# Optimization experiments

Measured on AMD Instinct MI355X. Metric: run time of the kernel, lower is better.

Reference implementation:

```python
import jax, jax.numpy as jnp
import numpy as np

B, S, D = 2, 2048, 1024
H, A = 16, 64  # num_heads, attention_dim


def setup_inputs() -> dict:
    key = jax.random.key(0)
    ks = jax.random.split(key, 9)
    sd = D ** -0.5
    so = (H * A) ** -0.5
    return {
        "x": jax.random.normal(ks[0], (B, S, D), dtype=jnp.float32),
        "Wq": jax.random.normal(ks[1], (D, H * A), dtype=jnp.float32) * sd,
        "bq": jnp.zeros((H * A,), dtype=jnp.float32),
        "Wk": jax.random.normal(ks[2], (D, H * A), dtype=jnp.float32) * sd,
        "bk": jnp.zeros((H * A,), dtype=jnp.float32),
        "Wv": jax.random.normal(ks[3], (D, H * A), dtype=jnp.float32) * sd,
        "bv": jnp.zeros((H * A,), dtype=jnp.float32),
        "Wo": jax.random.normal(ks[4], (H * A, D), dtype=jnp.float32) * so,
        "bo": jnp.zeros((D,), dtype=jnp.float32),
    }


def reference(x, Wq, bq, Wk, bk, Wv, bv, Wo, bo):
    b, s, _ = x.shape
    # project and split heads: [b, s, H, A]
    q = (x @ Wq + bq).reshape(b, s, H, A)
    k = (x @ Wk + bk).reshape(b, s, H, A)
    v = (x @ Wv + bv).reshape(b, s, H, A)
    # scores [b, H, s, s]
    scores = jnp.einsum("bqhd,bkhd->bhqk", q, k) / jnp.sqrt(jnp.float32(A))
    weights = jax.nn.softmax(scores, axis=-1)
    attended = jnp.einsum("bhqk,bkhd->bqhd", weights, v).reshape(b, s, H * A)
    return attended @ Wo + bo
```

## Files before the change

### kernel.cpp

```cpp
#include <hip/hip_runtime.h>
#include <hip/hip_bf16.h>

typedef __attribute__((ext_vector_type(8))) short bf16x8;
typedef __attribute__((ext_vector_type(4))) float f32x4;

#define LOG2E 1.44269504088896f

extern "C" __device__ float __ocml_native_exp2_f32(float);

__device__ __forceinline__ unsigned short f2bf(float f) {
    union { float f; unsigned int u; } v; v.f = f;
    unsigned int r = v.u + 0x7FFF + ((v.u >> 16) & 1);
    return (unsigned short)(r >> 16);
}

__device__ __forceinline__ unsigned int pk_bf16(float lo, float hi) {
    unsigned int r;
    asm("v_cvt_pk_bf16_f32 %0, %1, %2" : "=v"(r) : "v"(lo), "v"(hi));
    return r;
}

typedef __attribute__((address_space(3))) unsigned int lds_uint;
typedef __attribute__((address_space(1))) const unsigned int glob_uint;
__device__ __forceinline__ void gl2lds16(const void* g, void* l) {
    __builtin_amdgcn_global_load_lds((glob_uint*)g, (lds_uint*)l, 16, 0, 0);
}

#define SYNC(vm)                                                             \
    asm volatile("s_waitcnt vmcnt(" #vm ")\n\ts_waitcnt lgkmcnt(0)" ::: "memory"); \
    __builtin_amdgcn_s_barrier();                                            \
    asm volatile("" ::: "memory")

__global__ __launch_bounds__(256) void cvt_bf16(const float* __restrict__ in,
                                                unsigned int* __restrict__ out, int n4) {
    int i = blockIdx.x * 256 + threadIdx.x;
    if (i >= n4) return;
    float4 v = ((const float4*)in)[i];
    uint2 o;
    o.x = pk_bf16(v.x, v.y);
    o.y = pk_bf16(v.z, v.w);
    ((uint2*)out)[i] = o;
}

__global__ __launch_bounds__(256) void transpose4_bf16(
    const float* __restrict__ w0, const float* __restrict__ w1,
    const float* __restrict__ w2, const float* __restrict__ w3,
    unsigned short* __restrict__ o0, unsigned short* __restrict__ o1,
    unsigned short* __restrict__ o2, unsigned short* __restrict__ o3) {
    const int z = blockIdx.z;
    const float* in = (z == 0) ? w0 : (z == 1) ? w1 : (z == 2) ? w2 : w3;
    unsigned short* out = (z == 0) ? o0 : (z == 1) ? o1 : (z == 2) ? o2 : o3;
    __shared__ float t[32][33];
    int tx = threadIdx.x & 31, ty = threadIdx.x >> 5;
    int r0 = blockIdx.y * 32, c0 = blockIdx.x * 32;
    for (int i = 0; i < 32; i += 8)
        t[ty + i][tx] = in[(size_t)(r0 + ty + i) * 1024 + c0 + tx];
    __syncthreads();
    for (int i = 0; i < 32; i += 8)
        out[(size_t)(c0 + ty + i) * 1024 + r0 + tx] = f2bf(t[tx][ty + i]);
}

__device__ __forceinline__ void gemm_core(const short* __restrict__ A,
                                          const short* __restrict__ BT,
                                          int K, int bm0, int bn0,
                                          short* sm, f32x4 acc[4][4]) {
    const int tid = threadIdx.x;
    const int lane = tid & 63;
    const int w = tid >> 6;
    const int wr0 = (w >> 1) * 64;
    const int wc0 = (w & 1) * 64;
    const int l15 = lane & 15, quad = lane >> 4;
    const int sr = lane >> 2;
    const int slog = (lane & 3) ^ (sr & 3) ^ (sr >> 2);

#pragma unroll
    for (int i = 0; i < 4; i++)
#pragma unroll
        for (int j = 0; j < 4; j++) acc[i][j] = (f32x4)0.f;

    const short* sp[4];
    int sdo[4];
#pragma unroll
    for (int i = 0; i < 4; i++) {
        int c = w * 4 + i;
        sp[i] = (c < 8) ? A + (size_t)(bm0 + c * 16 + sr) * K + slog * 8
                        : BT + (size_t)(bn0 + (c - 8) * 16 + sr) * K + slog * 8;
        sdo[i] = c * 512;
    }
    auto stage = [&](int buf) {
        short* bb = sm + buf * 8192;
#pragma unroll
        for (int i = 0; i < 4; i++) {
            gl2lds16(sp[i], bb + sdo[i]);
            sp[i] += 32;
        }
    };
    const int ph = (quad ^ (l15 & 3) ^ (l15 >> 2)) * 8;
    auto loadf = [&](bf16x8* af, bf16x8* bfr, int buf) {
        const short* Ab = sm + buf * 8192;
        const short* Bb = Ab + 4096;
#pragma unroll
        for (int im = 0; im < 4; im++)
            af[im] = *(const bf16x8*)&Ab[(wr0 + im * 16 + l15) * 32 + ph];
#pragma unroll
        for (int in = 0; in < 4; in++)
            bfr[in] = *(const bf16x8*)&Bb[(wc0 + in * 16 + l15) * 32 + ph];
        __builtin_amdgcn_sched_barrier(0);
    };
    auto computef = [&](const bf16x8* af, const bf16x8* bfr) {
        __builtin_amdgcn_s_setprio(1);
#pragma unroll
        for (int im = 0; im < 4; im++)
#pragma unroll
            for (int in = 0; in < 4; in++)
                acc[im][in] = __builtin_amdgcn_mfma_f32_16x16x32_bf16(af[im], bfr[in], acc[im][in], 0, 0, 0);
        __builtin_amdgcn_s_setprio(0);
    };

    stage(0); stage(1);
    asm volatile("s_waitcnt vmcnt(4)" ::: "memory");
    __builtin_amdgcn_s_barrier();
    asm volatile("" ::: "memory");

    bf16x8 aA[4], bA[4], aB[4], bB[4];
    loadf(aA, bA, 0);

    const int nt = K >> 5;
    int bs = 2, rb = 1;
    for (int t = 0; t < nt - 2; t += 2) {
        stage(bs); bs = (bs == 2) ? 0 : bs + 1;
        SYNC(4);
        loadf(aB, bB, rb); rb = (rb == 2) ? 0 : rb + 1;
        computef(aA, bA);
        stage(bs); bs = (bs == 2) ? 0 : bs + 1;
        SYNC(4);
        loadf(aA, bA, rb); rb = (rb == 2) ? 0 : rb + 1;
        computef(aB, bB);
    }
    SYNC(0);
    loadf(aB, bB, rb);
    computef(aA, bA);
    computef(aB, bB);
}

__global__ __launch_bounds__(256, 3) void gemm_qkv(
    const short* __restrict__ xb,
    const short* __restrict__ wqT, const short* __restrict__ wkT, const short* __restrict__ wvT,
    const float* __restrict__ bq, const float* __restrict__ bk, const float* __restrict__ bv,
    unsigned short* __restrict__ qb, unsigned short* __restrict__ kb, unsigned short* __restrict__ vTb) {
    __shared__ short sm[24576];
    const int z = blockIdx.z;
    const short* Amat = (z == 2) ? wvT : xb;
    const short* Bmat = (z == 0) ? wqT : (z == 1) ? wkT : xb;
    const float* bias = (z == 0) ? bq : (z == 1) ? bk : bv;
    const float scl = (z == 0) ? 0.125f * LOG2E : 1.f;
    const int bm0 = (z == 2) ? blockIdx.y * 128 : blockIdx.x * 128;
    const int bn0 = (z == 2) ? blockIdx.x * 128 : blockIdx.y * 128;
    f32x4 acc[4][4];
    gemm_core(Amat, Bmat, 1024, bm0, bn0, sm, acc);
    const int lane = threadIdx.x & 63, w = threadIdx.x >> 6;
    const int wr0 = (w >> 1) * 64, wc0 = (w & 1) * 64, l15 = lane & 15, quad = lane >> 4;
    if (z == 2) {
        for (int im = 0; im < 4; im++)
            for (int in = 0; in < 4; in++)
                for (int r = 0; r < 4; r++) {
                    int rowa = bm0 + wr0 + im * 16 + quad * 4 + r;
                    int colg = bn0 + wc0 + in * 16 + l15;
                    unsigned short ov = f2bf(acc[im][in][r] + bias[rowa]);
                    int b = colg >> 11, s = colg & 2047;
                    vTb[(size_t)b * 2097152 + (size_t)rowa * 2048 + s] = ov;
                }
    } else {
        for (int im = 0; im < 4; im++)
            for (int in = 0; in < 4; in++)
                for (int r = 0; r < 4; r++) {
                    int rowg = bm0 + wr0 + im * 16 + quad * 4 + r;
                    int colg = bn0 + wc0 + in * 16 + l15;
                    unsigned short ov = f2bf((acc[im][in][r] + bias[colg]) * scl);
                    int b = rowg >> 11, s = rowg & 2047;
                    int h = colg >> 6, a = colg & 63;
                    int bh = b * 16 + h;
                    if (z == 0) qb[((size_t)bh * 2048 + s) * 64 + a] = ov;
                    else        kb[((size_t)bh * 2048 + s) * 64 + a] = ov;
                }
    }
}

__global__ __launch_bounds__(256, 3) void gemm_out(
    const short* __restrict__ att, const short* __restrict__ woT,
    const float* __restrict__ bo, float* __restrict__ out) {
    __shared__ short sm[24576];
    const int bm0 = blockIdx.x * 128, bn0 = blockIdx.y * 128;
    f32x4 acc[4][4];
    gemm_core(att, woT, 1024, bm0, bn0, sm, acc);
    const int lane = threadIdx.x & 63, w = threadIdx.x >> 6;
    const int wr0 = (w >> 1) * 64, wc0 = (w & 1) * 64, l15 = lane & 15, quad = lane >> 4;
    for (int im = 0; im < 4; im++)
        for (int in = 0; in < 4; in++)
            for (int r = 0; r < 4; r++) {
                int rowg = bm0 + wr0 + im * 16 + quad * 4 + r;
                int colg = bn0 + wc0 + in * 16 + l15;
                out[(size_t)rowg * 1024 + colg] = acc[im][in][r] + bo[colg];
            }
}

__global__ __launch_bounds__(256, 2) void flash_attn(
    const unsigned short* __restrict__ qb, const unsigned short* __restrict__ kb,
    const unsigned short* __restrict__ vTb, unsigned short* __restrict__ att) {
    __shared__ short Ks[4][4096];
    __shared__ short Vs[4][4096];
    const int tid = threadIdx.x, lane = tid & 63, w = tid >> 6;
    const int l15 = lane & 15, quad = lane >> 4;
    const int q0 = blockIdx.x * 128;
    const int bh = blockIdx.y;
    const size_t qkbase = (size_t)bh * 2048 * 64;
    const size_t vbase = (size_t)bh * 64 * 2048;
    const int sr = lane >> 3;
    const int slog = (lane & 7) ^ sr;
    const int l7 = l15 & 7;

    const unsigned short* sgp;
    int sgstep, sgr;
    short* sgb;
    if (w < 2) {
        sgp = kb + qkbase + (size_t)(w * 32 + sr) * 64 + slog * 8;
        sgstep = 4096; sgr = 512;
        sgb = &Ks[0][0] + w * 2048;
    } else {
        sgp = vTb + vbase + (size_t)((w - 2) * 32 + sr) * 2048 + slog * 8;
        sgstep = 64; sgr = 16384;
        sgb = &Vs[0][0] + (w - 2) * 2048;
    }
    auto stage_tile = [&](int buf) {
        short* sd = sgb + buf * 4096;
        gl2lds16(sgp, sd);
        gl2lds16(sgp + sgr, sd + 512);
        gl2lds16(sgp + 2 * sgr, sd + 1024);
        gl2lds16(sgp + 3 * sgr, sd + 1536);
        sgp += sgstep;
    };

    const int wq0 = w * 32;
    const int c0 = (quad ^ l7) * 8, c1 = c0 ^ 32;
    const int fb = l15 * 64;

    const unsigned short* qrow = qb + qkbase + (size_t)(q0 + wq0 + l15) * 64 + quad * 8;
    bf16x8 aq00 = *(const bf16x8*)qrow;
    bf16x8 aq01 = *(const bf16x8*)(qrow + 32);
    bf16x8 aq10 = *(const bf16x8*)(qrow + 1024);
    bf16x8 aq11 = *(const bf16x8*)(qrow + 1024 + 32);

    stage_tile(0); stage_tile(1); stage_tile(2);
    asm volatile("s_waitcnt vmcnt(8)" ::: "memory");
    __builtin_amdgcn_s_barrier();
    asm volatile("" ::: "memory");

    f32x4 o0[4], o1[4];
#pragma unroll
    for (int dt = 0; dt < 4; dt++) { o0[dt] = (f32x4)0.f; o1[dt] = (f32x4)0.f; }
    f32x4 ls0 = (f32x4)0.f, ls1 = (f32x4)0.f;

    auto load_frags = [&](bf16x8* kf, bf16x8* vf, int buf) {
        const short* Kb = &Ks[0][0] + buf * 4096;
        const short* Vb = &Vs[0][0] + buf * 4096;
#pragma unroll
        for (int t = 0; t < 4; t++) {
            kf[2 * t]     = *(const bf16x8*)(Kb + fb + c0 + t * 1024);
            kf[2 * t + 1] = *(const bf16x8*)(Kb + fb + c1 + t * 1024);
            vf[2 * t]     = *(const bf16x8*)(Vb + fb + c0 + t * 1024);
            vf[2 * t + 1] = *(const bf16x8*)(Vb + fb + c1 + t * 1024);
        }
        __builtin_amdgcn_sched_barrier(0);
    };

    auto smax = [&](f32x4 (&sc)[4], f32x4& lsr, bf16x8 (&bp)[2]) {
#pragma unroll
        for (int t = 0; t < 4; t++) {
#pragma unroll
            for (int r = 0; r < 4; r++) sc[t][r] = __ocml_native_exp2_f32(sc[t][r]);
            lsr += sc[t];
        }
#pragma unroll
        for (int t2 = 0; t2 < 2; t2++) {
            unsigned pa = pk_bf16(sc[2 * t2][0], sc[2 * t2][1]);
            unsigned pb = pk_bf16(sc[2 * t2][2], sc[2 * t2][3]);
            unsigned pc = pk_bf16(sc[2 * t2 + 1][0], sc[2 * t2 + 1][1]);
            unsigned pd = pk_bf16(sc[2 * t2 + 1][2], sc[2 * t2 + 1][3]);
            asm("v_permlane32_swap_b32 %0, %1" : "+v"(pa), "+v"(pc));
            asm("v_permlane32_swap_b32 %0, %1" : "+v"(pb), "+v"(pd));
            asm("v_permlane16_swap_b32 %0, %1" : "+v"(pa), "+v"(pc));
            asm("v_permlane16_swap_b32 %0, %1" : "+v"(pb), "+v"(pd));
            union { unsigned u[4]; bf16x8 v; } cvt;
            cvt.u[0] = pa; cvt.u[1] = pb; cvt.u[2] = pc; cvt.u[3] = pd;
            bp[t2] = cvt.v;
        }
    };

    auto compute_step = [&](const bf16x8* kf, const bf16x8* vf) {
        f32x4 sc0[4], sc1[4];
        __builtin_amdgcn_s_setprio(1);
#pragma unroll
        for (int t = 0; t < 4; t++) {
            sc0[t] = __builtin_amdgcn_mfma_f32_16x16x32_bf16(kf[2 * t], aq00, (f32x4)0.f, 0, 0, 0);
            sc1[t] = __builtin_amdgcn_mfma_f32_16x16x32_bf16(kf[2 * t], aq10, (f32x4)0.f, 0, 0, 0);
        }
#pragma unroll
        for (int t = 0; t < 4; t++) {
            sc0[t] = __builtin_amdgcn_mfma_f32_16x16x32_bf16(kf[2 * t + 1], aq01, sc0[t], 0, 0, 0);
            sc1[t] = __builtin_amdgcn_mfma_f32_16x16x32_bf16(kf[2 * t + 1], aq11, sc1[t], 0, 0, 0);
        }
        __builtin_amdgcn_s_setprio(0);
        bf16x8 bp0[2], bp1[2];
        smax(sc0, ls0, bp0);
        smax(sc1, ls1, bp1);
        __builtin_amdgcn_s_setprio(1);
#pragma unroll
        for (int t2 = 0; t2 < 2; t2++)
#pragma unroll
            for (int dt = 0; dt < 4; dt++) {
                o0[dt] = __builtin_amdgcn_mfma_f32_16x16x32_bf16(vf[2 * dt + t2], bp0[t2], o0[dt], 0, 0, 0);
                o1[dt] = __builtin_amdgcn_mfma_f32_16x16x32_bf16(vf[2 * dt + t2], bp1[t2], o1[dt], 0, 0, 0);
            }
        __builtin_amdgcn_s_setprio(0);
    };

    bf16x8 kA[8], vA[8], kB[8], vB[8];
    load_frags(kA, vA, 0);

    for (int t = 0; t < 28; t += 2) {
        stage_tile((t + 3) & 3);
        SYNC(8);
        load_frags(kB, vB, (t + 1) & 3);
        compute_step(kA, vA);
        stage_tile((t + 4) & 3);
        SYNC(8);
        load_frags(kA, vA, (t + 2) & 3);
        compute_step(kB, vB);
    }
    stage_tile(3);
    SYNC(8);
    load_frags(kB, vB, 29 & 3);
    compute_step(kA, vA);
    SYNC(4);
    load_frags(kA, vA, 30 & 3);
    compute_step(kB, vB);
    SYNC(0);
    load_frags(kB, vB, 31 & 3);
    compute_step(kA, vA);
    compute_step(kB, vB);

    const int b = bh >> 4, h = bh & 15;
    float l0 = (ls0[0] + ls0[1]) + (ls0[2] + ls0[3]);
    l0 += __shfl_xor(l0, 16);
    l0 += __shfl_xor(l0, 32);
    float inv0 = 1.f / l0;
    float l1 = (ls1[0] + ls1[1]) + (ls1[2] + ls1[3]);
    l1 += __shfl_xor(l1, 16);
    l1 += __shfl_xor(l1, 32);
    float inv1 = 1.f / l1;
    int s = q0 + wq0 + l15;
#pragma unroll
    for (int dt = 0; dt < 4; dt++) {
        int col = h * 64 + dt * 16 + quad * 4;
        uint2 pk;
        pk.x = pk_bf16(o0[dt][0] * inv0, o0[dt][1] * inv0);
        pk.y = pk_bf16(o0[dt][2] * inv0, o0[dt][3] * inv0);
        *(uint2*)&att[((size_t)b * 2048 + s) * 1024 + col] = pk;
        pk.x = pk_bf16(o1[dt][0] * inv1, o1[dt][1] * inv1);
        pk.y = pk_bf16(o1[dt][2] * inv1, o1[dt][3] * inv1);
        *(uint2*)&att[((size_t)b * 2048 + s + 16) * 1024 + col] = pk;
    }
}

extern "C" void kernel_launch(void* const* d_in, const int* in_sizes, int n_in,
                              void* d_out, int out_size, void* d_ws, size_t ws_size,
                              hipStream_t stream) {
    const float* x  = (const float*)d_in[0];
    const float* Wq = (const float*)d_in[1];
    const float* bq = (const float*)d_in[2];
    const float* Wk = (const float*)d_in[3];
    const float* bk = (const float*)d_in[4];
    const float* Wv = (const float*)d_in[5];
    const float* bv = (const float*)d_in[6];
    const float* Wo = (const float*)d_in[7];
    const float* bo = (const float*)d_in[8];
    float* out = (float*)d_out;

    short* ws  = (short*)d_ws;
    short* xb  = ws;
    short* wqT = ws + 4 * 1024 * 1024;
    short* wkT = wqT + 1024 * 1024;
    short* wvT = wkT + 1024 * 1024;
    short* woT = wvT + 1024 * 1024;
    short* qb  = woT + 1024 * 1024;
    short* kb  = qb + 4 * 1024 * 1024;
    short* vTb = kb + 4 * 1024 * 1024;
    short* att = vTb + 4 * 1024 * 1024;

    cvt_bf16<<<4096, 256, 0, stream>>>(x, (unsigned int*)xb, 1024 * 1024);
    transpose4_bf16<<<dim3(32, 32, 4), 256, 0, stream>>>(
        Wq, Wk, Wv, Wo,
        (unsigned short*)wqT, (unsigned short*)wkT,
        (unsigned short*)wvT, (unsigned short*)woT);
    gemm_qkv<<<dim3(32, 8, 3), 256, 0, stream>>>(xb, wqT, wkT, wvT, bq, bk, bv,
                                                 (unsigned short*)qb, (unsigned short*)kb,
                                                 (unsigned short*)vTb);
    flash_attn<<<dim3(16, 32), 256, 0, stream>>>((const unsigned short*)qb,
                                                 (const unsigned short*)kb,
                                                 (const unsigned short*)vTb,
                                                 (unsigned short*)att);
    gemm_out<<<dim3(32, 8), 256, 0, stream>>>(att, woT, bo, out);
}
```

Before: 181.5 us.

## Software-pipeline flash attention across tiles and remap blocks for XCD locality

Restructures the flash-attention main loop so the PV MFMA of the previous tile runs after the QK and softmax of the current tile, with K and V fragment loads split and issued at different points. This overlaps exp and softmax VALU work with matrix-core work and LDS reads. The launch is flattened to a 1D grid, and block IDs are remapped so blocks sharing the same batch-head land on the same XCD, aiming for better L2 reuse of K and V. It adds register pressure from the extra P buffers and relies on hand-tuned waitcnt and barrier placement.

Measured after the change: 178.0 us. About the same (-1.9%).

```diff
diff --git a/kernel.cpp b/kernel.cpp
--- a/kernel.cpp
+++ b/kernel.cpp
@@ -211,8 +211,9 @@
     __shared__ short Vs[4][4096];
     const int tid = threadIdx.x, lane = tid & 63, w = tid >> 6;
     const int l15 = lane & 15, quad = lane >> 4;
-    const int q0 = blockIdx.x * 128;
-    const int bh = blockIdx.y;
+    const int lid = ((blockIdx.x & 7) << 6) | (blockIdx.x >> 3);
+    const int q0 = (lid & 15) * 128;
+    const int bh = lid >> 4;
     const size_t qkbase = (size_t)bh * 2048 * 64;
     const size_t vbase = (size_t)bh * 64 * 2048;
     const int sr = lane >> 3;
@@ -251,7 +252,7 @@
     bf16x8 aq11 = *(const bf16x8*)(qrow + 1024 + 32);
 
     stage_tile(0); stage_tile(1); stage_tile(2);
-    asm volatile("s_waitcnt vmcnt(8)" ::: "memory");
+    asm volatile("s_waitcnt vmcnt(4)" ::: "memory");
     __builtin_amdgcn_s_barrier();
     asm volatile("" ::: "memory");
 
@@ -260,20 +261,40 @@
     for (int dt = 0; dt < 4; dt++) { o0[dt] = (f32x4)0.f; o1[dt] = (f32x4)0.f; }
     f32x4 ls0 = (f32x4)0.f, ls1 = (f32x4)0.f;
 
-    auto load_frags = [&](bf16x8* kf, bf16x8* vf, int buf) {
+    auto load_kf = [&](bf16x8* kf, int buf) {
         const short* Kb = &Ks[0][0] + buf * 4096;
-        const short* Vb = &Vs[0][0] + buf * 4096;
 #pragma unroll
         for (int t = 0; t < 4; t++) {
             kf[2 * t]     = *(const bf16x8*)(Kb + fb + c0 + t * 1024);
             kf[2 * t + 1] = *(const bf16x8*)(Kb + fb + c1 + t * 1024);
+        }
+    };
+    bf16x8 vf[8];
+    auto load_vf = [&](int buf) {
+        const short* Vb = &Vs[0][0] + buf * 4096;
+#pragma unroll
+        for (int t = 0; t < 4; t++) {
             vf[2 * t]     = *(const bf16x8*)(Vb + fb + c0 + t * 1024);
             vf[2 * t + 1] = *(const bf16x8*)(Vb + fb + c1 + t * 1024);
         }
-        __builtin_amdgcn_sched_barrier(0);
-    };
-
-    auto smax = [&](f32x4 (&sc)[4], f32x4& lsr, bf16x8 (&bp)[2]) {
+    };
+
+    auto qk = [&](const bf16x8* kf, f32x4* sc0, f32x4* sc1) {
+        __builtin_amdgcn_s_setprio(1);
+#pragma unroll
+        for (int t = 0; t < 4; t++) {
+            sc0[t] = __builtin_amdgcn_mfma_f32_16x16x32_bf16(kf[2 * t], aq00, (f32x4)0.f, 0, 0, 0);
+            sc1[t] = __builtin_amdgcn_mfma_f32_16x16x32_bf16(kf[2 * t], aq10, (f32x4)0.f, 0, 0, 0);
+        }
+#pragma unroll
+        for (int t = 0; t < 4; t++) {
+            sc0[t] = __builtin_amdgcn_mfma_f32_16x16x32_bf16(kf[2 * t + 1], aq01, sc0[t], 0, 0, 0);
+            sc1[t] = __builtin_amdgcn_mfma_f32_16x16x32_bf16(kf[2 * t + 1], aq11, sc1[t], 0, 0, 0);
+        }
+        __builtin_amdgcn_s_setprio(0);
+    };
+
+    auto smax = [&](f32x4 (&sc)[4], f32x4& lsr, bf16x8* bp) {
 #pragma unroll
         for (int t = 0; t < 4; t++) {
 #pragma unroll
@@ -296,58 +317,48 @@
         }
     };
 
-    auto compute_step = [&](const bf16x8* kf, const bf16x8* vf) {
-        f32x4 sc0[4], sc1[4];
+    auto pv = [&](const bf16x8* bp) {
         __builtin_amdgcn_s_setprio(1);
 #pragma unroll
-        for (int t = 0; t < 4; t++) {
-            sc0[t] = __builtin_amdgcn_mfma_f32_16x16x32_bf16(kf[2 * t], aq00, (f32x4)0.f, 0, 0, 0);
-            sc1[t] = __builtin_amdgcn_mfma_f32_16x16x32_bf16(kf[2 * t], aq10, (f32x4)0.f, 0, 0, 0);
-        }
-#pragma unroll
-        for (int t = 0; t < 4; t++) {
-            sc0[t] = __builtin_amdgcn_mfma_f32_16x16x32_bf16(kf[2 * t + 1], aq01, sc0[t], 0, 0, 0);
-            sc1[t] = __builtin_amdgcn_mfma_f32_16x16x32_bf16(kf[2 * t + 1], aq11, sc1[t], 0, 0, 0);
-        }
-        __builtin_amdgcn_s_setprio(0);
-        bf16x8 bp0[2], bp1[2];
-        smax(sc0, ls0, bp0);
-        smax(sc1, ls1, bp1);
-        __builtin_amdgcn_s_setprio(1);
-#pragma unroll
         for (int t2 = 0; t2 < 2; t2++)
 #pragma unroll
             for (int dt = 0; dt < 4; dt++) {
-                o0[dt] = __builtin_amdgcn_mfma_f32_16x16x32_bf16(vf[2 * dt + t2], bp0[t2], o0[dt], 0, 0, 0);
-                o1[dt] = __builtin_amdgcn_mfma_f32_16x16x32_bf16(vf[2 * dt + t2], bp1[t2], o1[dt], 0, 0, 0);
+                o0[dt] = __builtin_amdgcn_mfma_f32_16x16x32_bf16(vf[2 * dt + t2], bp[t2], o0[dt], 0, 0, 0);
+                o1[dt] = __builtin_amdgcn_mfma_f32_16x16x32_bf16(vf[2 * dt + t2], bp[2 + t2], o1[dt], 0, 0, 0);
             }
         __builtin_amdgcn_s_setprio(0);
     };
 
-    bf16x8 kA[8], vA[8], kB[8], vB[8];
-    load_frags(kA, vA, 0);
-
-    for (int t = 0; t < 28; t += 2) {
-        stage_tile((t + 3) & 3);
-        SYNC(8);
-        load_frags(kB, vB, (t + 1) & 3);
-        compute_step(kA, vA);
-        stage_tile((t + 4) & 3);
-        SYNC(8);
-        load_frags(kA, vA, (t + 2) & 3);
-        compute_step(kB, vB);
-    }
-    stage_tile(3);
-    SYNC(8);
-    load_frags(kB, vB, 29 & 3);
-    compute_step(kA, vA);
-    SYNC(4);
-    load_frags(kA, vA, 30 & 3);
-    compute_step(kB, vB);
-    SYNC(0);
-    load_frags(kB, vB, 31 & 3);
-    compute_step(kA, vA);
-    compute_step(kB, vB);
+    bf16x8 kfA[8], kfB[8];
+    bf16x8 bpA[4], bpB[4];
+
+    load_kf(kfA, 0);
+    asm volatile("s_waitcnt lgkmcnt(0)" ::: "memory");
+    __builtin_amdgcn_sched_barrier(0);
+
+    auto step = [&](int t, const bf16x8* kfC, bf16x8* kfN, bf16x8* bpC,
+                    const bf16x8* bpP, bool dokf, bool dopv, bool dostage) {
+        if (dokf) load_kf(kfN, (t + 1) & 3);
+        __builtin_amdgcn_sched_barrier(0);
+        f32x4 sc0[4], sc1[4];
+        qk(kfC, sc0, sc1);
+        smax(sc0, ls0, bpC);
+        smax(sc1, ls1, bpC + 2);
+        if (dopv) pv(bpP);
+        load_vf(t & 3);
+        if (dostage) stage_tile((t + 3) & 3);
+    };
+
+    step(0, kfA, kfB, bpA, bpB, true, false, true); SYNC(4);
+    for (int t = 1; t < 29; t += 2) {
+        step(t,     kfB, kfA, bpB, bpA, true, true, true); SYNC(4);
+        step(t + 1, kfA, kfB, bpA, bpB, true, true, true); SYNC(4);
+    }
+    step(29, kfB, kfA, bpB, bpA, true, true, false); SYNC(0);
+    step(30, kfA, kfB, bpA, bpB, true, true, false); SYNC(0);
+    step(31, kfB, kfA, bpB, bpA, false, true, false);
+    asm volatile("s_waitcnt lgkmcnt(0)" ::: "memory");
+    pv(bpB);
 
     const int b = bh >> 4, h = bh & 15;
     float l0 = (ls0[0] + ls0[1]) + (ls0[2] + ls0[3]);
@@ -405,9 +416,9 @@
     gemm_qkv<<<dim3(32, 8, 3), 256, 0, stream>>>(xb, wqT, wkT, wvT, bq, bk, bv,
                                                  (unsigned short*)qb, (unsigned short*)kb,
                                                  (unsigned short*)vTb);
-    flash_attn<<<dim3(16, 32), 256, 0, stream>>>((const unsigned short*)qb,
-                                                 (const unsigned short*)kb,
-                                                 (const unsigned short*)vTb,
-                                                 (unsigned short*)att);
+    flash_attn<<<512, 256, 0, stream>>>((const unsigned short*)qb,
+                                        (const unsigned short*)kb,
+                                        (const unsigned short*)vTb,
+                                        (unsigned short*)att);
     gemm_out<<<dim3(32, 8), 256, 0, stream>>>(att, woT, bo, out);
 }
```
